# Kernel tuning notes

Measured on AMD Instinct MI355X. Metric: run time of the kernel, lower is better.

## Reference

```python
import jax, jax.numpy as jnp
import numpy as np

EPS = 1e-12

def l2norm(v, axis):
    return v / jnp.maximum(jnp.linalg.norm(v, axis=axis, keepdims=True), EPS)

def setup_inputs() -> dict:
    key = jax.random.key(0)
    k1, k2, k3, k4 = jax.random.split(key, 4)
    N, C, S, K = 16, 128, 16384, 64
    return {
        "x": jax.random.normal(k1, (N, C, S), dtype=jnp.float32),
        "fc_w": jax.random.normal(k2, (K, C), dtype=jnp.float32),
        "fc_b": jax.random.normal(k3, (K,), dtype=jnp.float32),
        "centroids": jax.random.uniform(k4, (K, C), dtype=jnp.float32),
    }

def reference(x, fc_w, fc_b, centroids):
    # x: [N, C, S]; fc_w: [K, C]; centroids: [K, C]
    x = l2norm(x, axis=1)  # descriptor-wise L2 normalize over channels
    # 1x1 conv (per-position linear) -> soft assignment over clusters
    logits = jnp.einsum('ncs,kc->nks', x, fc_w) + fc_b[None, :, None]
    soft = jax.nn.softmax(logits, axis=1)  # [N, K, S]
    # vlad[n,k,c] = sum_s soft[n,k,s] * (x[n,c,s] - centroids[k,c])
    # matmul decomposition avoids materializing [N,K,C,S]
    a_sum = soft.sum(axis=-1)  # [N, K]
    vlad = jnp.einsum('nks,ncs->nkc', soft, x) - a_sum[:, :, None] * centroids[None]
    vlad = l2norm(vlad, axis=2)            # intra-normalization
    vlad = vlad.reshape(vlad.shape[0], -1)  # [N, K*C]
    vlad = l2norm(vlad, axis=1)            # final L2 normalize
    return vlad
```

## Files before the change

kernel.cpp:

```cpp
#include <hip/hip_runtime.h>
#include <hip/hip_fp16.h>

#define N_ 16
#define C_ 128
#define S_ 16384
#define K_ 64

typedef __attribute__((ext_vector_type(4))) float f32x4;
typedef __attribute__((ext_vector_type(8))) _Float16 f16x8;
typedef __attribute__((ext_vector_type(4))) _Float16 f16x4;

#define SWZ_S(s) ((((s) ^ ((s) >> 3)) & 7) << 3)
#define SWZ16(k) (((k) & 7) << 3)
#define SWZ8(r) (((r) & 7) << 3)

static __device__ __forceinline__ unsigned int pack_fp8x4(float a, float b,
                                                          float c, float d) {
    int v = __builtin_amdgcn_cvt_pk_fp8_f32(a, b, 0, false);
    v = __builtin_amdgcn_cvt_pk_fp8_f32(c, d, v, true);
    return (unsigned int)v;
}

__global__ __launch_bounds__(256, 3) void fused_kernel(
    const float* __restrict__ x, const float* __restrict__ fc_w,
    const float* __restrict__ fc_b, __half* __restrict__ vlad_part,
    float* __restrict__ a_part)
{
    __shared__ __align__(16) _Float16 xT[64 * 128];
    __shared__ __align__(16) _Float16 Wlds[64 * 128];
    __shared__ __align__(16) unsigned char xC8[2][128 * 64];
    __shared__ __align__(16) unsigned char sst8[64 * 64];
    __shared__ float rns[2][64];

    const int tid = threadIdx.x;
    const int lane = tid & 63, w = tid >> 6;
    const int lr = lane & 15, g = lane >> 4;
    const int fsw8 = SWZ8(lr);
    const int fsw16 = SWZ16(lr);

    const int b = blockIdx.x;
    const int n     = (b < 256) ? (b >> 4) : ((b - 256) >> 5);
    const int lo    = (b < 256) ? (b & 15) * 6 : 96 + ((b - 256) & 31) * 5;
    const int cnt   = (b < 256) ? 6 : 5;
    const int jslot = (b < 256) ? (b & 15) : 16 + ((b - 256) & 31);
    const int sl    = n * 48 + jslot;

#pragma unroll
    for (int i = 0; i < 8; ++i) {
        int idx = i * 256 + tid;
        int c4 = idx & 31, k = idx >> 5;
        float4 wv = *(const float4*)(fc_w + k * C_ + c4 * 4);
        f16x4 hi = {(_Float16)wv.x, (_Float16)wv.y, (_Float16)wv.z, (_Float16)wv.w};
        *(f16x4*)&Wlds[k * 128 + ((c4 * 4) ^ SWZ16(k))] = hi;
    }
    if (tid < 128) (&rns[0][0])[tid] = 0.f;

    float bias[4];
#pragma unroll
    for (int nt = 0; nt < 4; ++nt) bias[nt] = fc_b[nt * 16 + lr];
    float a_acc[4] = {0.f, 0.f, 0.f, 0.f};
    f32x4 vacc[8];
#pragma unroll
    for (int nt = 0; nt < 8; ++nt) vacc[nt] = (f32x4){0.f, 0.f, 0.f, 0.f};
    f32x4 accp[4];

    const float* xb = x + (size_t)n * C_ * S_;
    const int s4 = tid & 15;
    int cqv[2];
#pragma unroll
    for (int i = 0; i < 2; ++i) cqv[i] = i * 16 + (tid >> 4);

    float4 pre[2][4];
#pragma unroll
    for (int i = 0; i < 2; ++i)
#pragma unroll
        for (int cc = 0; cc < 4; ++cc)
            pre[i][cc] = *(const float4*)(xb + (size_t)(cqv[i] * 4 + cc) * S_ +
                                          lo * 64 + s4 * 4);

    auto softmax_emit = [&](int pit) {
        float rnl[4], ai[4];
#pragma unroll
        for (int r = 0; r < 4; ++r)
            rnl[r] = 1.0f / fmaxf(sqrtf(rns[pit][w * 16 + g * 4 + r]), 1e-12f);
        if (lane < 16) rns[pit][w * 16 + lane] = 0.f;
#pragma unroll
        for (int nt = 0; nt < 4; ++nt)
#pragma unroll
            for (int r = 0; r < 4; ++r)
                accp[nt][r] = __expf(accp[nt][r] * rnl[r] + bias[nt]);
#pragma unroll
        for (int r = 0; r < 4; ++r) {
            float sum = (accp[0][r] + accp[1][r]) + (accp[2][r] + accp[3][r]);
            sum += __shfl_xor(sum, 1);
            sum += __shfl_xor(sum, 2);
            sum += __shfl_xor(sum, 4);
            sum += __shfl_xor(sum, 8);
            float bi = 1.0f / sum;
            ai[r] = bi * rnl[r] * 256.0f;
#pragma unroll
            for (int nt = 0; nt < 4; ++nt) a_acc[nt] += accp[nt][r] * bi;
        }
#pragma unroll
        for (int nt = 0; nt < 4; ++nt) {
            int k = nt * 16 + lr;
            int sloc = w * 16 + g * 4;
            unsigned int pk = pack_fp8x4(accp[nt][0] * ai[0], accp[nt][1] * ai[1],
                                         accp[nt][2] * ai[2], accp[nt][3] * ai[3]);
            *(unsigned int*)&sst8[k * 64 + (sloc ^ SWZ8(k))] = pk;
        }
    };

#pragma unroll 1
    for (int it = 0; it < cnt; ++it) {
        const int bb = it & 1;
        __syncthreads();

        float part[4] = {0.f, 0.f, 0.f, 0.f};
#pragma unroll
        for (int i = 0; i < 2; ++i) {
            int cq = cqv[i];
#pragma unroll
            for (int jj = 0; jj < 4; ++jj) {
                float v0 = (&pre[i][0].x)[jj], v1 = (&pre[i][1].x)[jj],
                      v2 = (&pre[i][2].x)[jj], v3 = (&pre[i][3].x)[jj];
                part[jj] += v0 * v0 + v1 * v1 + v2 * v2 + v3 * v3;
                f16x4 p = {(_Float16)v0, (_Float16)v1, (_Float16)v2, (_Float16)v3};
                int s = s4 * 4 + jj;
                *(f16x4*)&xT[s * 128 + ((cq * 4) ^ SWZ_S(s))] = p;
            }
#pragma unroll
            for (int cc = 0; cc < 4; ++cc) {
                int c = cq * 4 + cc;
                unsigned int pk = pack_fp8x4(pre[i][cc].x, pre[i][cc].y,
                                             pre[i][cc].z, pre[i][cc].w);
                *(unsigned int*)&xC8[bb][c * 64 + ((s4 * 4) ^ SWZ8(c))] = pk;
            }
        }
#pragma unroll
        for (int jj = 0; jj < 4; ++jj) {
            part[jj] += __shfl_xor(part[jj], 16);
            part[jj] += __shfl_xor(part[jj], 32);
        }
        if (g == 0) {
#pragma unroll
            for (int jj = 0; jj < 4; ++jj)
                atomicAdd(&rns[it & 1][lr * 4 + jj], part[jj]);
        }
        if (it > 0) softmax_emit((it - 1) & 1);
        if (it + 1 < cnt) {
            const float* xb2 = xb + (lo + it + 1) * 64;
#pragma unroll
            for (int i = 0; i < 2; ++i)
#pragma unroll
                for (int cc = 0; cc < 4; ++cc)
                    pre[i][cc] = *(const float4*)(xb2 + (size_t)(cqv[i] * 4 + cc) * S_ + s4 * 4);
        }
        __syncthreads();

#pragma unroll
        for (int nt = 0; nt < 4; ++nt) accp[nt] = (f32x4){0.f, 0.f, 0.f, 0.f};
        __builtin_amdgcn_s_setprio(1);
#pragma unroll
        for (int kt = 0; kt < 4; ++kt) {
            const int co = kt * 32 + g * 8;
            const int sa = w * 16 + lr;
            f16x8 af = *(const f16x8*)&xT[sa * 128 + (co ^ SWZ_S(sa))];
#pragma unroll
            for (int nt = 0; nt < 4; ++nt) {
                f16x8 wf = *(const f16x8*)&Wlds[(nt * 16 + lr) * 128 + (co ^ fsw16)];
                accp[nt] = __builtin_amdgcn_mfma_f32_16x16x32_f16(af, wf, accp[nt], 0, 0, 0);
            }
        }
        if (it > 0) {
            const unsigned char* xcp = xC8[bb ^ 1];
#pragma unroll
            for (int kt = 0; kt < 2; ++kt) {
                const int so = kt * 32 + g * 8;
                long pa = *(const long*)&sst8[(w * 16 + lr) * 64 + (so ^ fsw8)];
#pragma unroll
                for (int nt = 0; nt < 8; ++nt) {
                    long xv = *(const long*)&xcp[(nt * 16 + lr) * 64 + (so ^ fsw8)];
                    vacc[nt] = __builtin_amdgcn_mfma_f32_16x16x32_fp8_fp8(pa, xv, vacc[nt], 0, 0, 0);
                }
            }
        }
        __builtin_amdgcn_s_setprio(0);
    }

    const int lastb = (cnt - 1) & 1;
    __syncthreads();
    softmax_emit(lastb);
    __syncthreads();
    {
        const unsigned char* xcp = xC8[lastb];
#pragma unroll
        for (int kt = 0; kt < 2; ++kt) {
            const int so = kt * 32 + g * 8;
            long pa = *(const long*)&sst8[(w * 16 + lr) * 64 + (so ^ fsw8)];
#pragma unroll
            for (int nt = 0; nt < 8; ++nt) {
                long xv = *(const long*)&xcp[(nt * 16 + lr) * 64 + (so ^ fsw8)];
                vacc[nt] = __builtin_amdgcn_mfma_f32_16x16x32_fp8_fp8(pa, xv, vacc[nt], 0, 0, 0);
            }
        }
    }

    __half* vp = vlad_part + (size_t)sl * (K_ * C_) + (w * 16) * C_;
#pragma unroll
    for (int nt = 0; nt < 8; ++nt)
#pragma unroll
        for (int r = 0; r < 4; ++r)
            vp[(g * 4 + r) * C_ + nt * 16 + lr] =
                __float2half(vacc[nt][r] * (1.0f / 256.0f));
#pragma unroll
    for (int nt = 0; nt < 4; ++nt) {
        a_acc[nt] += __shfl_xor(a_acc[nt], 16);
        a_acc[nt] += __shfl_xor(a_acc[nt], 32);
    }
    if (lane < 16) {
#pragma unroll
        for (int nt = 0; nt < 4; ++nt)
            a_part[sl * 256 + w * 64 + nt * 16 + lr] = a_acc[nt];
    }
}

__global__ __launch_bounds__(1024) void finalize_kernel(
    const __half* __restrict__ vlad_part, const float* __restrict__ a_part,
    const float* __restrict__ centroids, float* __restrict__ out)
{
    __shared__ float red[16];
    const int n = blockIdx.x;
    const int t = threadIdx.x;
    const int k = t >> 4, q = t & 15;
    const int c0 = q * 8;

    float vsum[8] = {0.f, 0.f, 0.f, 0.f, 0.f, 0.f, 0.f, 0.f};
    {
        const __half* p = vlad_part + (size_t)(n * 48) * (K_ * C_) + k * C_ + c0;
#pragma unroll 4
        for (int slb = 0; slb < 48; ++slb) {
            f16x8 v = *(const f16x8*)(p + (size_t)slb * (K_ * C_));
#pragma unroll
            for (int jj = 0; jj < 8; ++jj) vsum[jj] += (float)v[jj];
        }
    }

    float av = 0.f;
#pragma unroll
    for (int cc = 0; cc < 3; ++cc) {
        int ch = q * 3 + cc;
        const float* ap = a_part + (size_t)(n * 48 + ch) * 256 + k;
#pragma unroll
        for (int ww = 0; ww < 4; ++ww) av += ap[ww * 64];
    }
    av += __shfl_xor(av, 1);
    av += __shfl_xor(av, 2);
    av += __shfl_xor(av, 4);
    av += __shfl_xor(av, 8);

    const float* cp = centroids + k * C_ + c0;
    float4 cpa = *(const float4*)cp;
    float4 cpb = *(const float4*)(cp + 4);
    float v[8];
    float ssq = 0.f;
#pragma unroll
    for (int jj = 0; jj < 8; ++jj) {
        float cv = (jj < 4) ? (&cpa.x)[jj] : (&cpb.x)[jj - 4];
        float val = vsum[jj] - av * cv;
        v[jj] = val;
        ssq += val * val;
    }
    ssq += __shfl_xor(ssq, 1);
    ssq += __shfl_xor(ssq, 2);
    ssq += __shfl_xor(ssq, 4);
    ssq += __shfl_xor(ssq, 8);
    const float inv1 = 1.0f / fmaxf(sqrtf(ssq), 1e-12f);

    float gp = (q == 0) ? ssq * inv1 * inv1 : 0.f;
#pragma unroll
    for (int off = 1; off < 64; off <<= 1) gp += __shfl_xor(gp, off);
    if ((t & 63) == 0) red[t >> 6] = gp;
    __syncthreads();
    float G = 0.f;
#pragma unroll
    for (int i = 0; i < 16; ++i) G += red[i];
    const float ginv = 1.0f / fmaxf(sqrtf(G), 1e-12f);

    float* op = out + (size_t)n * (K_ * C_) + k * C_ + c0;
    float4 oa, ob;
#pragma unroll
    for (int jj = 0; jj < 4; ++jj) {
        (&oa.x)[jj] = v[jj] * inv1 * ginv;
        (&ob.x)[jj] = v[jj + 4] * inv1 * ginv;
    }
    *(float4*)op = oa;
    *(float4*)(op + 4) = ob;
}

extern "C" void kernel_launch(void* const* d_in, const int* in_sizes, int n_in,
                              void* d_out, int out_size, void* d_ws, size_t ws_size,
                              hipStream_t stream) {
    const float* x     = (const float*)d_in[0];
    const float* fc_w  = (const float*)d_in[1];
    const float* fc_b  = (const float*)d_in[2];
    const float* cent  = (const float*)d_in[3];
    float* out = (float*)d_out;

    char* ws = (char*)d_ws;
    __half* vlad_part = (__half*)ws;
    float* a_part     = (float*)(ws + (size_t)768 * K_ * C_ * 2);

    fused_kernel<<<768, 256, 0, stream>>>(x, fc_w, fc_b, vlad_part, a_part);
    finalize_kernel<<<N_, 1024, 0, stream>>>(vlad_part, a_part, cent, out);
}
```

Baseline: 53.01 us.

## Split fused kernel into producer and VLAD warp groups in 512-thread blocks

Doubles the block size to 512 threads and specializes the two halves. The front 256 threads do the fp16 transpose, norm, logits MFMA and softmax. The back 256 threads pack fp8 x and run the VLAD fp8 MFMA accumulation on the previous tile. The soft-assignment buffer is double-buffered so the two stages can overlap across iterations, and the grid becomes a uniform 512 blocks of 8 tiles each instead of the uneven 6/5 split, which cuts the partials the finalize kernel must reduce. Both halves load x redundantly, adding global/L2 traffic, and the larger blocks may lower occupancy.

```diff
diff --git a/kernel.cpp b/kernel.cpp
--- a/kernel.cpp
+++ b/kernel.cpp
@@ -21,7 +21,7 @@
     return (unsigned int)v;
 }
 
-__global__ __launch_bounds__(256, 3) void fused_kernel(
+__global__ __launch_bounds__(512, 4) void fused_kernel(
     const float* __restrict__ x, const float* __restrict__ fc_w,
     const float* __restrict__ fc_b, __half* __restrict__ vlad_part,
     float* __restrict__ a_part)
@@ -29,25 +29,22 @@
     __shared__ __align__(16) _Float16 xT[64 * 128];
     __shared__ __align__(16) _Float16 Wlds[64 * 128];
     __shared__ __align__(16) unsigned char xC8[2][128 * 64];
-    __shared__ __align__(16) unsigned char sst8[64 * 64];
+    __shared__ __align__(16) unsigned char sst8[2][64 * 64];
     __shared__ float rns[2][64];
 
     const int tid = threadIdx.x;
-    const int lane = tid & 63, w = tid >> 6;
+    const int b = blockIdx.x;
+    const int n = b >> 5, chunk = b & 31;
+    const int lane = tid & 63, w = (tid >> 6) & 3;
     const int lr = lane & 15, g = lane >> 4;
+    const bool front = tid < 256;
+    const int rt = tid & 255;
     const int fsw8 = SWZ8(lr);
     const int fsw16 = SWZ16(lr);
 
-    const int b = blockIdx.x;
-    const int n     = (b < 256) ? (b >> 4) : ((b - 256) >> 5);
-    const int lo    = (b < 256) ? (b & 15) * 6 : 96 + ((b - 256) & 31) * 5;
-    const int cnt   = (b < 256) ? 6 : 5;
-    const int jslot = (b < 256) ? (b & 15) : 16 + ((b - 256) & 31);
-    const int sl    = n * 48 + jslot;
-
-#pragma unroll
-    for (int i = 0; i < 8; ++i) {
-        int idx = i * 256 + tid;
+#pragma unroll
+    for (int i = 0; i < 4; ++i) {
+        int idx = i * 512 + tid;
         int c4 = idx & 31, k = idx >> 5;
         float4 wv = *(const float4*)(fc_w + k * C_ + c4 * 4);
         f16x4 hi = {(_Float16)wv.x, (_Float16)wv.y, (_Float16)wv.z, (_Float16)wv.w};
@@ -65,18 +62,16 @@
     f32x4 accp[4];
 
     const float* xb = x + (size_t)n * C_ * S_;
-    const int s4 = tid & 15;
-    int cqv[2];
-#pragma unroll
-    for (int i = 0; i < 2; ++i) cqv[i] = i * 16 + (tid >> 4);
+    const int s4 = rt & 15;
+    const int cq0 = rt >> 4;
 
     float4 pre[2][4];
 #pragma unroll
     for (int i = 0; i < 2; ++i)
 #pragma unroll
         for (int cc = 0; cc < 4; ++cc)
-            pre[i][cc] = *(const float4*)(xb + (size_t)(cqv[i] * 4 + cc) * S_ +
-                                          lo * 64 + s4 * 4);
+            pre[i][cc] = *(const float4*)(xb + (size_t)((i * 16 + cq0) * 4 + cc) * S_ +
+                                          chunk * 512 + s4 * 4);
 
     auto softmax_emit = [&](int pit) {
         float rnl[4], ai[4];
@@ -107,121 +102,140 @@
             int sloc = w * 16 + g * 4;
             unsigned int pk = pack_fp8x4(accp[nt][0] * ai[0], accp[nt][1] * ai[1],
                                          accp[nt][2] * ai[2], accp[nt][3] * ai[3]);
-            *(unsigned int*)&sst8[k * 64 + (sloc ^ SWZ8(k))] = pk;
+            *(unsigned int*)&sst8[pit][k * 64 + (sloc ^ SWZ8(k))] = pk;
         }
     };
 
 #pragma unroll 1
-    for (int it = 0; it < cnt; ++it) {
+    for (int it = 0; it < 8; ++it) {
         const int bb = it & 1;
         __syncthreads();
 
-        float part[4] = {0.f, 0.f, 0.f, 0.f};
-#pragma unroll
-        for (int i = 0; i < 2; ++i) {
-            int cq = cqv[i];
+        if (front) {
+            float part[4] = {0.f, 0.f, 0.f, 0.f};
+#pragma unroll
+            for (int i = 0; i < 2; ++i) {
+                int cq = i * 16 + cq0;
+#pragma unroll
+                for (int jj = 0; jj < 4; ++jj) {
+                    float v0 = (&pre[i][0].x)[jj], v1 = (&pre[i][1].x)[jj],
+                          v2 = (&pre[i][2].x)[jj], v3 = (&pre[i][3].x)[jj];
+                    part[jj] += v0 * v0 + v1 * v1 + v2 * v2 + v3 * v3;
+                    f16x4 p = {(_Float16)v0, (_Float16)v1, (_Float16)v2, (_Float16)v3};
+                    int s = s4 * 4 + jj;
+                    *(f16x4*)&xT[s * 128 + ((cq * 4) ^ SWZ_S(s))] = p;
+                }
+            }
 #pragma unroll
             for (int jj = 0; jj < 4; ++jj) {
-                float v0 = (&pre[i][0].x)[jj], v1 = (&pre[i][1].x)[jj],
-                      v2 = (&pre[i][2].x)[jj], v3 = (&pre[i][3].x)[jj];
-                part[jj] += v0 * v0 + v1 * v1 + v2 * v2 + v3 * v3;
-                f16x4 p = {(_Float16)v0, (_Float16)v1, (_Float16)v2, (_Float16)v3};
-                int s = s4 * 4 + jj;
-                *(f16x4*)&xT[s * 128 + ((cq * 4) ^ SWZ_S(s))] = p;
-            }
-#pragma unroll
-            for (int cc = 0; cc < 4; ++cc) {
-                int c = cq * 4 + cc;
-                unsigned int pk = pack_fp8x4(pre[i][cc].x, pre[i][cc].y,
-                                             pre[i][cc].z, pre[i][cc].w);
-                *(unsigned int*)&xC8[bb][c * 64 + ((s4 * 4) ^ SWZ8(c))] = pk;
-            }
-        }
-#pragma unroll
-        for (int jj = 0; jj < 4; ++jj) {
-            part[jj] += __shfl_xor(part[jj], 16);
-            part[jj] += __shfl_xor(part[jj], 32);
-        }
-        if (g == 0) {
-#pragma unroll
-            for (int jj = 0; jj < 4; ++jj)
-                atomicAdd(&rns[it & 1][lr * 4 + jj], part[jj]);
-        }
-        if (it > 0) softmax_emit((it - 1) & 1);
-        if (it + 1 < cnt) {
-            const float* xb2 = xb + (lo + it + 1) * 64;
-#pragma unroll
-            for (int i = 0; i < 2; ++i)
-#pragma unroll
-                for (int cc = 0; cc < 4; ++cc)
-                    pre[i][cc] = *(const float4*)(xb2 + (size_t)(cqv[i] * 4 + cc) * S_ + s4 * 4);
+                part[jj] += __shfl_xor(part[jj], 16);
+                part[jj] += __shfl_xor(part[jj], 32);
+            }
+            if (g == 0) {
+#pragma unroll
+                for (int jj = 0; jj < 4; ++jj)
+                    atomicAdd(&rns[bb][lr * 4 + jj], part[jj]);
+            }
+            if (it > 0) softmax_emit(bb ^ 1);
+            if (it < 7) {
+                const float* xb2 = xb + chunk * 512 + (it + 1) * 64;
+#pragma unroll
+                for (int i = 0; i < 2; ++i)
+#pragma unroll
+                    for (int cc = 0; cc < 4; ++cc)
+                        pre[i][cc] = *(const float4*)(xb2 + (size_t)((i * 16 + cq0) * 4 + cc) * S_ + s4 * 4);
+            }
+        } else {
+#pragma unroll
+            for (int i = 0; i < 2; ++i) {
+                int cq = i * 16 + cq0;
+#pragma unroll
+                for (int cc = 0; cc < 4; ++cc) {
+                    int c = cq * 4 + cc;
+                    unsigned int pk = pack_fp8x4(pre[i][cc].x, pre[i][cc].y,
+                                                 pre[i][cc].z, pre[i][cc].w);
+                    *(unsigned int*)&xC8[bb][c * 64 + ((s4 * 4) ^ SWZ8(c))] = pk;
+                }
+            }
+            if (it < 7) {
+                const float* xb2 = xb + chunk * 512 + (it + 1) * 64;
+#pragma unroll
+                for (int i = 0; i < 2; ++i)
+#pragma unroll
+                    for (int cc = 0; cc < 4; ++cc)
+                        pre[i][cc] = *(const float4*)(xb2 + (size_t)((i * 16 + cq0) * 4 + cc) * S_ + s4 * 4);
+            }
         }
         __syncthreads();
 
-#pragma unroll
-        for (int nt = 0; nt < 4; ++nt) accp[nt] = (f32x4){0.f, 0.f, 0.f, 0.f};
-        __builtin_amdgcn_s_setprio(1);
-#pragma unroll
-        for (int kt = 0; kt < 4; ++kt) {
-            const int co = kt * 32 + g * 8;
-            const int sa = w * 16 + lr;
-            f16x8 af = *(const f16x8*)&xT[sa * 128 + (co ^ SWZ_S(sa))];
-#pragma unroll
-            for (int nt = 0; nt < 4; ++nt) {
-                f16x8 wf = *(const f16x8*)&Wlds[(nt * 16 + lr) * 128 + (co ^ fsw16)];
-                accp[nt] = __builtin_amdgcn_mfma_f32_16x16x32_f16(af, wf, accp[nt], 0, 0, 0);
-            }
-        }
-        if (it > 0) {
+        if (front) {
+#pragma unroll
+            for (int nt = 0; nt < 4; ++nt) accp[nt] = (f32x4){0.f, 0.f, 0.f, 0.f};
+            __builtin_amdgcn_s_setprio(1);
+#pragma unroll
+            for (int kt = 0; kt < 4; ++kt) {
+                const int co = kt * 32 + g * 8;
+                const int sa = w * 16 + lr;
+                f16x8 af = *(const f16x8*)&xT[sa * 128 + (co ^ SWZ_S(sa))];
+#pragma unroll
+                for (int nt = 0; nt < 4; ++nt) {
+                    f16x8 wf = *(const f16x8*)&Wlds[(nt * 16 + lr) * 128 + (co ^ fsw16)];
+                    accp[nt] = __builtin_amdgcn_mfma_f32_16x16x32_f16(af, wf, accp[nt], 0, 0, 0);
+                }
+            }
+            __builtin_amdgcn_s_setprio(0);
+        } else if (it > 0) {
             const unsigned char* xcp = xC8[bb ^ 1];
+            const unsigned char* ssp = sst8[bb ^ 1];
+            __builtin_amdgcn_s_setprio(1);
 #pragma unroll
             for (int kt = 0; kt < 2; ++kt) {
                 const int so = kt * 32 + g * 8;
-                long pa = *(const long*)&sst8[(w * 16 + lr) * 64 + (so ^ fsw8)];
+                long pa = *(const long*)&ssp[(w * 16 + lr) * 64 + (so ^ fsw8)];
 #pragma unroll
                 for (int nt = 0; nt < 8; ++nt) {
                     long xv = *(const long*)&xcp[(nt * 16 + lr) * 64 + (so ^ fsw8)];
                     vacc[nt] = __builtin_amdgcn_mfma_f32_16x16x32_fp8_fp8(pa, xv, vacc[nt], 0, 0, 0);
                 }
             }
-        }
-        __builtin_amdgcn_s_setprio(0);
-    }
-
-    const int lastb = (cnt - 1) & 1;
+            __builtin_amdgcn_s_setprio(0);
+        }
+    }
+
     __syncthreads();
-    softmax_emit(lastb);
+    if (front) softmax_emit(1);
     __syncthreads();
-    {
-        const unsigned char* xcp = xC8[lastb];
+    if (front) {
+#pragma unroll
+        for (int nt = 0; nt < 4; ++nt) {
+            a_acc[nt] += __shfl_xor(a_acc[nt], 16);
+            a_acc[nt] += __shfl_xor(a_acc[nt], 32);
+        }
+        if (lane < 16) {
+#pragma unroll
+            for (int nt = 0; nt < 4; ++nt)
+                a_part[b * 256 + w * 64 + nt * 16 + lr] = a_acc[nt];
+        }
+    } else {
+        const unsigned char* xcp = xC8[1];
+        const unsigned char* ssp = sst8[1];
 #pragma unroll
         for (int kt = 0; kt < 2; ++kt) {
             const int so = kt * 32 + g * 8;
-            long pa = *(const long*)&sst8[(w * 16 + lr) * 64 + (so ^ fsw8)];
+            long pa = *(const long*)&ssp[(w * 16 + lr) * 64 + (so ^ fsw8)];
 #pragma unroll
             for (int nt = 0; nt < 8; ++nt) {
                 long xv = *(const long*)&xcp[(nt * 16 + lr) * 64 + (so ^ fsw8)];
                 vacc[nt] = __builtin_amdgcn_mfma_f32_16x16x32_fp8_fp8(pa, xv, vacc[nt], 0, 0, 0);
             }
         }
-    }
-
-    __half* vp = vlad_part + (size_t)sl * (K_ * C_) + (w * 16) * C_;
-#pragma unroll
-    for (int nt = 0; nt < 8; ++nt)
-#pragma unroll
-        for (int r = 0; r < 4; ++r)
-            vp[(g * 4 + r) * C_ + nt * 16 + lr] =
-                __float2half(vacc[nt][r] * (1.0f / 256.0f));
-#pragma unroll
-    for (int nt = 0; nt < 4; ++nt) {
-        a_acc[nt] += __shfl_xor(a_acc[nt], 16);
-        a_acc[nt] += __shfl_xor(a_acc[nt], 32);
-    }
-    if (lane < 16) {
-#pragma unroll
-        for (int nt = 0; nt < 4; ++nt)
-            a_part[sl * 256 + w * 64 + nt * 16 + lr] = a_acc[nt];
+        __half* vp = vlad_part + (size_t)b * (K_ * C_) + (w * 16) * C_;
+#pragma unroll
+        for (int nt = 0; nt < 8; ++nt)
+#pragma unroll
+            for (int r = 0; r < 4; ++r)
+                vp[(g * 4 + r) * C_ + nt * 16 + lr] =
+                    __float2half(vacc[nt][r] * (1.0f / 256.0f));
     }
 }
 
@@ -237,9 +251,9 @@
 
     float vsum[8] = {0.f, 0.f, 0.f, 0.f, 0.f, 0.f, 0.f, 0.f};
     {
-        const __half* p = vlad_part + (size_t)(n * 48) * (K_ * C_) + k * C_ + c0;
+        const __half* p = vlad_part + (size_t)(n * 32) * (K_ * C_) + k * C_ + c0;
 #pragma unroll 4
-        for (int slb = 0; slb < 48; ++slb) {
+        for (int slb = 0; slb < 32; ++slb) {
             f16x8 v = *(const f16x8*)(p + (size_t)slb * (K_ * C_));
 #pragma unroll
             for (int jj = 0; jj < 8; ++jj) vsum[jj] += (float)v[jj];
@@ -248,9 +262,9 @@
 
     float av = 0.f;
 #pragma unroll
-    for (int cc = 0; cc < 3; ++cc) {
-        int ch = q * 3 + cc;
-        const float* ap = a_part + (size_t)(n * 48 + ch) * 256 + k;
+    for (int cc = 0; cc < 2; ++cc) {
+        int ch = q * 2 + cc;
+        const float* ap = a_part + (size_t)(n * 32 + ch) * 256 + k;
 #pragma unroll
         for (int ww = 0; ww < 4; ++ww) av += ap[ww * 64];
     }
@@ -309,8 +323,8 @@
 
     char* ws = (char*)d_ws;
     __half* vlad_part = (__half*)ws;
-    float* a_part     = (float*)(ws + (size_t)768 * K_ * C_ * 2);
-
-    fused_kernel<<<768, 256, 0, stream>>>(x, fc_w, fc_b, vlad_part, a_part);
+    float* a_part     = (float*)(ws + (size_t)512 * K_ * C_ * 2);
+
+    fused_kernel<<<512, 512, 0, stream>>>(x, fc_w, fc_b, vlad_part, a_part);
     finalize_kernel<<<N_, 1024, 0, stream>>>(vlad_part, a_part, cent, out);
 }
```

After: 68.69 us. 29.6% more time.
